# Kernel optimization log

Measured on AMD Instinct MI355X. Metric: run time of the kernel, lower is better.

Reference implementation:

```python
import jax, jax.numpy as jnp
import numpy as np

B, T, S, E, H, F = 4, 1024, 1024, 512, 8, 2048
D = E // H  # head_dim = 64
SCALE = D ** -0.5
EPS = 1e-5


def setup_inputs() -> dict:
    key = jax.random.key(0)
    ks = jax.random.split(key, 16)
    w = lambda k, shape: jax.random.normal(k, shape, jnp.float32) * 0.02
    inp = {
        'tgt': jax.random.normal(ks[0], (B, T, E), jnp.float32),
        'memory': jax.random.normal(ks[1], (B, S, E), jnp.float32),
    }
    for i, n in enumerate(['sWq', 'sWk', 'sWv', 'sWo', 'cWq', 'cWk', 'cWv', 'cWo']):
        inp[n] = w(ks[2 + i], (E, E))
    for n in ['sbq', 'sbk', 'sbv', 'sbo', 'cbq', 'cbk', 'cbv', 'cbo']:
        inp[n] = jnp.zeros((E,), jnp.float32)
    inp['fW1'] = w(ks[10], (E, F)); inp['fb1'] = jnp.zeros((F,), jnp.float32)
    inp['fW2'] = w(ks[11], (F, E)); inp['fb2'] = jnp.zeros((E,), jnp.float32)
    for n in ['g1', 'g2', 'g3']:
        inp[n] = jnp.ones((E,), jnp.float32)
    for n in ['be1', 'be2', 'be3']:
        inp[n] = jnp.zeros((E,), jnp.float32)
    return inp


def _ln(x, g, b):
    mu = jnp.mean(x, axis=-1, keepdims=True)
    var = jnp.mean(jnp.square(x - mu), axis=-1, keepdims=True)
    return (x - mu) * jax.lax.rsqrt(var + EPS) * g + b


def _mha(xq, xkv, Wq, bq, Wk, bk, Wv, bv, Wo, bo):
    # dense-equivalent of full N^2 edge-list attention (softmax over source nodes per target)
    Bq, Tq, _ = xq.shape
    Skv = xkv.shape[1]
    q = (xq @ Wq + bq).reshape(Bq, Tq, H, D)
    k = (xkv @ Wk + bk).reshape(Bq, Skv, H, D)
    v = (xkv @ Wv + bv).reshape(Bq, Skv, H, D)
    scores = jnp.einsum('bthd,bshd->bhts', q, k) * SCALE
    wts = jax.nn.softmax(scores, axis=-1)
    out = jnp.einsum('bhts,bshd->bthd', wts, v).reshape(Bq, Tq, E)
    return out @ Wo + bo


def reference(tgt, memory,
              sWq, sbq, sWk, sbk, sWv, sbv, sWo, sbo,
              cWq, cbq, cWk, cbk, cWv, cbv, cWo, cbo,
              fW1, fb1, fW2, fb2,
              g1, be1, g2, be2, g3, be3):
    # post-norm decoder layer: self-attn -> cross-attn -> FFN (dropout=0 eval)
    x = _ln(tgt + _mha(tgt, tgt, sWq, sbq, sWk, sbk, sWv, sbv, sWo, sbo), g1, be1)
    x = _ln(x + _mha(x, memory, cWq, cbq, cWk, cbk, cWv, cbv, cWo, cbo), g2, be2)
    ff = jax.nn.relu(x @ fW1 + fb1) @ fW2 + fb2
    x = _ln(x + ff, g3, be3)
    return x
```

## Files before the change

### kernel.cpp

```cpp
#include <hip/hip_runtime.h>

typedef unsigned short ushort_t;
typedef short short8 __attribute__((ext_vector_type(8)));
typedef float float4v __attribute__((ext_vector_type(4)));

__device__ __forceinline__ float bf2f(ushort_t u) {
    union { unsigned int i; float f; } x; x.i = ((unsigned int)u) << 16; return x.f;
}
__device__ __forceinline__ ushort_t f2bf(float f) {
    unsigned int u = __float_as_uint(f);
    unsigned int r = (u + 0x7FFFu + ((u >> 16) & 1u)) >> 16;
    return (ushort_t)r;
}
__device__ __forceinline__ void store_out(float* p, float v) { *p = v; }
__device__ __forceinline__ void store_out(ushort_t* p, float v) { *p = f2bf(v); }

__device__ __forceinline__ void gll16(const ushort_t* g, ushort_t* l) {
    __builtin_amdgcn_global_load_lds(
        (const __attribute__((address_space(1))) void*)g,
        (__attribute__((address_space(3))) void*)l, 16, 0, 0);
}

__global__ void detect_dtype(const ushort_t* __restrict__ tgt, int* __restrict__ flag) {
    __shared__ int red[256];
    const int tid = threadIdx.x;
    int p = 0;
    for (int i = tid; i < 512; i += 256) {
        ushort_t u = tgt[i];
        int e = (u >> 7) & 0xFF;
        if (u == 0 || (e >= 100 && e <= 140)) ++p;
    }
    red[tid] = p; __syncthreads();
    for (int off = 128; off > 0; off >>= 1) {
        if (tid < off) red[tid] += red[tid + off];
        __syncthreads();
    }
    if (tid == 0) flag[0] = (red[0] >= 480) ? 1 : 0;
}

__global__ __launch_bounds__(256) void prep_all(
    const void* sWq, const void* sWk, const void* sWv, const void* sWo,
    const void* cWq, const void* cWk, const void* cWv, const void* cWo,
    const void* fW1, const void* fW2,
    const void* tgt, const void* mem,
    const void* sbq, const void* sbk, const void* sbv, const void* sbo,
    const void* cbq, const void* cbk, const void* cbv, const void* cbo,
    const void* fb1, const void* fb2,
    ushort_t* __restrict__ wb, ushort_t* __restrict__ tb, ushort_t* __restrict__ mb,
    float* __restrict__ pb, const int* __restrict__ dflag)
{
    const bool f32 = (dflag[0] == 0);
    const int tid = threadIdx.x;
    const int z = blockIdx.z;

    if (z < 10) {
        const void* src; ushort_t* dst; int Kd, Nd;
        switch (z) {
            case 0: src = sWq; dst = wb + 0;       Kd = 512;  Nd = 512;  break;
            case 1: src = sWk; dst = wb + 262144;  Kd = 512;  Nd = 512;  break;
            case 2: src = sWv; dst = wb + 524288;  Kd = 512;  Nd = 512;  break;
            case 3: src = sWo; dst = wb + 786432;  Kd = 512;  Nd = 512;  break;
            case 4: src = cWq; dst = wb + 1048576; Kd = 512;  Nd = 512;  break;
            case 5: src = cWk; dst = wb + 1310720; Kd = 512;  Nd = 512;  break;
            case 6: src = cWv; dst = wb + 1572864; Kd = 512;  Nd = 512;  break;
            case 7: src = cWo; dst = wb + 1835008; Kd = 512;  Nd = 512;  break;
            case 8: src = fW1; dst = wb + 2097152; Kd = 512;  Nd = 2048; break;
            default:src = fW2; dst = wb + 3145728; Kd = 2048; Nd = 512;  break;
        }
        const int k0 = blockIdx.x * 64, n0 = blockIdx.y * 64;
        if (k0 >= Kd || n0 >= Nd) return;
        __shared__ ushort_t T[64][65];
#pragma unroll
        for (int i = 0; i < 16; ++i) {
            int j = i * 256 + tid;
            int r = j >> 6, c = j & 63;
            float v = f32 ? ((const float*)src)[(size_t)(k0 + r) * Nd + n0 + c]
                          : bf2f(((const ushort_t*)src)[(size_t)(k0 + r) * Nd + n0 + c]);
            T[r][c] = f2bf(v);
        }
        __syncthreads();
#pragma unroll
        for (int i = 0; i < 16; ++i) {
            int j = i * 256 + tid;
            int n = j >> 6, k = j & 63;
            dst[(size_t)(n0 + n) * Kd + k0 + k] = T[k][n];
        }
        return;
    }

    const int bid = blockIdx.x * 32 + blockIdx.y;
    if (z < 12) {
        const void* src = (z == 10) ? tgt : mem;
        ushort_t* dst = (z == 10) ? tb : mb;
        const int i = (bid * 256 + tid) * 8;
        if (f32) {
            float4 v0 = *(const float4*)((const float*)src + i);
            float4 v1 = *(const float4*)((const float*)src + i + 4);
            ushort_t o[8] = { f2bf(v0.x), f2bf(v0.y), f2bf(v0.z), f2bf(v0.w),
                              f2bf(v1.x), f2bf(v1.y), f2bf(v1.z), f2bf(v1.w) };
            *(uint4*)(dst + i) = *(const uint4*)o;
        } else {
            *(uint4*)(dst + i) = *(const uint4*)((const ushort_t*)src + i);
        }
        return;
    }

    {
        const int i = bid * 256 + tid;
        if (bid >= 26 || i >= 6656) return;
        const void* src; int off;
        if      (i < 512)  { src = sbq; off = i; }
        else if (i < 1024) { src = sbk; off = i - 512; }
        else if (i < 1536) { src = sbv; off = i - 1024; }
        else if (i < 2048) { src = sbo; off = i - 1536; }
        else if (i < 2560) { src = cbq; off = i - 2048; }
        else if (i < 3072) { src = cbk; off = i - 2560; }
        else if (i < 3584) { src = cbv; off = i - 3072; }
        else if (i < 4096) { src = cbo; off = i - 3584; }
        else if (i < 6144) { src = fb1; off = i - 4096; }
        else               { src = fb2; off = i - 6144; }
        pb[i] = f32 ? ((const float*)src)[off] : bf2f(((const ushort_t*)src)[off]);
    }
}

template<typename OutT, bool RELU, int BN>
__global__ __launch_bounds__(256) void gemm_tn(
    const ushort_t* __restrict__ A1, const ushort_t* __restrict__ A2,
    int ySplit, int lda,
    const ushort_t* __restrict__ Wt, int ldw,
    const float* __restrict__ bias,
    OutT* __restrict__ C, int ldc, int K)
{
    constexpr int MI = (BN == 128) ? 4 : 2;
    __shared__ ushort_t As[2][128][32];
    __shared__ ushort_t Bs[2][BN][32];
    const int tid = threadIdx.x;
    const int wave = tid >> 6, lane = tid & 63;
    const int quad = lane >> 4, l16 = lane & 15;
    const int m0 = blockIdx.x * 128, n0 = blockIdx.y * BN;
    const int wm = (BN == 128) ? (wave >> 1) * 64 : wave * 32;
    const int wn = (BN == 128) ? (wave & 1) * 64 : 0;
    const ushort_t* A = (((int)blockIdx.y) < ySplit) ? A1 : A2;

    float4v acc[MI][4];
#pragma unroll
    for (int mi = 0; mi < MI; ++mi)
#pragma unroll
        for (int ni = 0; ni < 4; ++ni) {
            acc[mi][ni][0] = 0.f; acc[mi][ni][1] = 0.f;
            acc[mi][ni][2] = 0.f; acc[mi][ni][3] = 0.f;
        }

    const int srow = lane >> 2;
    const int scc  = lane & 3;
    const int sg   = (scc - (lane >> 3)) & 3;
    const ushort_t* aptr0 = A  + (size_t)(m0 + wave * 16 + srow) * lda + sg * 8;
    const ushort_t* aptr1 = A  + (size_t)(m0 + 64 + wave * 16 + srow) * lda + sg * 8;
    const ushort_t* bptr0 = Wt + (size_t)(n0 + wave * 16 + srow) * ldw + sg * 8;
    const ushort_t* bptr1 = Wt + (size_t)(n0 + 64 + wave * 16 + srow) * ldw + sg * 8;

    gll16(aptr0, &As[0][wave * 16][0]);
    gll16(aptr1, &As[0][64 + wave * 16][0]);
    gll16(bptr0, &Bs[0][wave * 16][0]);
    if (BN == 128) gll16(bptr1, &Bs[0][64 + wave * 16][0]);

    const int ca = ((quad + (l16 >> 1)) & 3) * 8;
    int cur = 0;
    for (int k0 = 0; k0 < K; k0 += 32) {
        __syncthreads();
        if (k0 + 32 < K) {
            const int nb = cur ^ 1, ko = k0 + 32;
            gll16(aptr0 + ko, &As[nb][wave * 16][0]);
            gll16(aptr1 + ko, &As[nb][64 + wave * 16][0]);
            gll16(bptr0 + ko, &Bs[nb][wave * 16][0]);
            if (BN == 128) gll16(bptr1 + ko, &Bs[nb][64 + wave * 16][0]);
        }
        short8 af[MI], bfr[4];
#pragma unroll
        for (int mi = 0; mi < MI; ++mi)
            af[mi] = *(const short8*)(&As[cur][wm + mi * 16 + l16][ca]);
#pragma unroll
        for (int ni = 0; ni < 4; ++ni)
            bfr[ni] = *(const short8*)(&Bs[cur][wn + ni * 16 + l16][ca]);
#pragma unroll
        for (int mi = 0; mi < MI; ++mi)
#pragma unroll
            for (int ni = 0; ni < 4; ++ni)
                acc[mi][ni] = __builtin_amdgcn_mfma_f32_16x16x32_bf16(
                    af[mi], bfr[ni], acc[mi][ni], 0, 0, 0);
        cur ^= 1;
    }

#pragma unroll
    for (int ni = 0; ni < 4; ++ni) {
        const int col = n0 + wn + ni * 16 + l16;
        const float bv = bias[col];
#pragma unroll
        for (int mi = 0; mi < MI; ++mi)
#pragma unroll
            for (int r = 0; r < 4; ++r) {
                const int row = m0 + wm + mi * 16 + quad * 4 + r;
                float v = acc[mi][ni][r] + bv;
                if (RELU) v = fmaxf(v, 0.f);
                store_out(&C[(size_t)row * ldc + col], v);
            }
    }
}

__global__ __launch_bounds__(512) void attn_mfma(ushort_t* __restrict__ QKV)
{
    const int S = 1536;
    __shared__ ushort_t PsA[64][72];
    __shared__ ushort_t PsB[64][72];
    __shared__ ushort_t Ks[2][64][72];
    __shared__ ushort_t Vt[2][64][72];

    const int tid  = threadIdx.x;
    const int w    = tid >> 6;
    const int g    = w >> 2;
    const int wq   = w & 3;
    const int lane = tid & 63;
    const int quad = lane >> 4, l16 = lane & 15;
    const int ht   = tid & 255;
    const int qt = blockIdx.x, bh = blockIdx.y;
    const int b = bh >> 3, h = bh & 7;
    const size_t rowQ = (size_t)b * 1024 + qt * 64;
    const size_t kv0  = (size_t)b * 1024;

    const int kr = ht >> 2, kc = (ht & 3) * 16;
    const int sp = ht >> 3, dc = (ht & 7) * 8;
    const int vr0 = sp * 2;
    const int vrg = vr0 >> 3, vrof = vr0 & 7;

    {
        const int r = tid >> 3, c = (tid & 7) * 8;
        *(uint4*)(&PsA[r][c]) = *(const uint4*)(QKV + (rowQ + r) * S + h * 64 + c);
    }
    __syncthreads();
    short8 qf[2];
    qf[0] = *(const short8*)(&PsA[wq * 16 + l16][quad * 8]);
    qf[1] = *(const short8*)(&PsA[wq * 16 + l16][32 + quad * 8]);
    ushort_t (* __restrict__ Ps)[72] = g ? PsB : PsA;

    const float CEXP = 0.125f * 1.44269504f;
    const float MREF = 16.0f * CEXP;
    float lsum[4];
    float4v oacc[4];
#pragma unroll
    for (int r = 0; r < 4; ++r) lsum[r] = 0.f;
#pragma unroll
    for (int n = 0; n < 4; ++n) { oacc[n][0]=0.f; oacc[n][1]=0.f; oacc[n][2]=0.f; oacc[n][3]=0.f; }

    uint4 kA, kB, vA, vB;
    {
        const size_t sr = kv0 + g * 64;
        const ushort_t* ksrc = QKV + (sr + kr) * S + 512 + h * 64 + kc;
        kA = *(const uint4*)(ksrc);
        kB = *(const uint4*)(ksrc + 8);
        const ushort_t* vsrc = QKV + (sr + vr0) * S + 1024 + h * 64 + dc;
        vA = *(const uint4*)(vsrc);
        vB = *(const uint4*)(vsrc + S);
    }

    for (int it = 0; it < 8; ++it) {
        __syncthreads();
        *(uint4*)(&Ks[g][kr][kc])     = kA;
        *(uint4*)(&Ks[g][kr][kc + 8]) = kB;
        {
            const ushort_t* ae = (const ushort_t*)&vA;
            const ushort_t* be = (const ushort_t*)&vB;
#pragma unroll
            for (int j = 0; j < 8; ++j) {
                const int d = dc + j;
                const int cc = (vrg ^ (d >> 4)) & 7;
                *(unsigned int*)(&Vt[g][d][cc * 8 + vrof]) =
                    (unsigned int)ae[j] | ((unsigned int)be[j] << 16);
            }
        }
        __syncthreads();
        if (it < 7) {
            const size_t sr = kv0 + (it + 1) * 128 + g * 64;
            const ushort_t* ksrc = QKV + (sr + kr) * S + 512 + h * 64 + kc;
            kA = *(const uint4*)(ksrc);
            kB = *(const uint4*)(ksrc + 8);
            const ushort_t* vsrc = QKV + (sr + vr0) * S + 1024 + h * 64 + dc;
            vA = *(const uint4*)(vsrc);
            vB = *(const uint4*)(vsrc + S);
        }

        float4v sc[4];
#pragma unroll
        for (int sb = 0; sb < 4; ++sb) {
            float4v z; z[0]=0.f; z[1]=0.f; z[2]=0.f; z[3]=0.f;
            short8 kf0 = *(const short8*)(&Ks[g][sb * 16 + l16][quad * 8]);
            short8 kf1 = *(const short8*)(&Ks[g][sb * 16 + l16][32 + quad * 8]);
            z = __builtin_amdgcn_mfma_f32_16x16x32_bf16(qf[0], kf0, z, 0, 0, 0);
            z = __builtin_amdgcn_mfma_f32_16x16x32_bf16(qf[1], kf1, z, 0, 0, 0);
            sc[sb] = z;
        }

#pragma unroll
        for (int sb = 0; sb < 4; ++sb)
#pragma unroll
            for (int r = 0; r < 4; ++r) {
                float p = exp2f(fmaf(sc[sb][r], CEXP, -MREF));
                lsum[r] += p;
                Ps[wq * 16 + quad * 4 + r][sb * 16 + l16] = f2bf(p);
            }

        short8 pf[2];
        pf[0] = *(const short8*)(&Ps[wq * 16 + l16][quad * 8]);
        pf[1] = *(const short8*)(&Ps[wq * 16 + l16][32 + quad * 8]);
#pragma unroll
        for (int n = 0; n < 4; ++n) {
#pragma unroll
            for (int kc2 = 0; kc2 < 2; ++kc2) {
                const int cc = ((kc2 * 4 + quad) ^ n) & 7;
                short8 vf = *(const short8*)(&Vt[g][n * 16 + l16][cc * 8]);
                oacc[n] = __builtin_amdgcn_mfma_f32_16x16x32_bf16(pf[kc2], vf, oacc[n], 0, 0, 0);
            }
        }
    }

#pragma unroll
    for (int msk = 1; msk < 16; msk <<= 1)
#pragma unroll
        for (int r = 0; r < 4; ++r) lsum[r] += __shfl_xor(lsum[r], msk);

    float* exch = (float*)&Ks[0][0][0];
    float* exl  = (float*)&Vt[0][0][0];
    __syncthreads();
    if (g == 1) {
#pragma unroll
        for (int n = 0; n < 4; ++n)
#pragma unroll
            for (int r = 0; r < 4; ++r)
                exch[((wq * 4 + n) * 4 + r) * 64 + lane] = oacc[n][r];
        if (l16 == 0)
#pragma unroll
            for (int r = 0; r < 4; ++r) exl[wq * 16 + quad * 4 + r] = lsum[r];
    }
    __syncthreads();
    if (g == 0) {
#pragma unroll
        for (int r = 0; r < 4; ++r) lsum[r] += exl[wq * 16 + quad * 4 + r];
        float inv[4];
#pragma unroll
        for (int r = 0; r < 4; ++r) inv[r] = 1.f / lsum[r];
#pragma unroll
        for (int n = 0; n < 4; ++n)
#pragma unroll
            for (int r = 0; r < 4; ++r) {
                float o = oacc[n][r] + exch[((wq * 4 + n) * 4 + r) * 64 + lane];
                const size_t row = rowQ + wq * 16 + quad * 4 + r;
                QKV[row * S + h * 64 + n * 16 + l16] = f2bf(o * inv[r]);
            }
    }
}

template<bool RES_EXT, bool DELTA_F32, bool OUT_FLAG>
__global__ __launch_bounds__(256) void ln_kernel(
    const void* __restrict__ res, const void* __restrict__ delta,
    const void* __restrict__ g, const void* __restrict__ be,
    void* __restrict__ out, const int* __restrict__ dflag)
{
    const int E = 512;
    const bool extf32 = (dflag[0] == 0);
    const int row = blockIdx.x, tid = threadIdx.x;
    const int wave = tid >> 6, lane = tid & 63;
    const size_t base = (size_t)row * E;
    const int i0 = tid, i1 = tid + 256;

    float r0, r1;
    if (RES_EXT && extf32) {
        r0 = ((const float*)res)[base + i0];
        r1 = ((const float*)res)[base + i1];
    } else {
        r0 = bf2f(((const ushort_t*)res)[base + i0]);
        r1 = bf2f(((const ushort_t*)res)[base + i1]);
    }
    float d0v, d1v;
    if (DELTA_F32) {
        d0v = ((const float*)delta)[base + i0];
        d1v = ((const float*)delta)[base + i1];
    } else {
        d0v = bf2f(((const ushort_t*)delta)[base + i0]);
        d1v = bf2f(((const ushort_t*)delta)[base + i1]);
    }
    float x0 = r0 + d0v, x1 = r1 + d1v;

    __shared__ float red8[8];
    float s = x0 + x1;
#pragma unroll
    for (int m = 1; m < 64; m <<= 1) s += __shfl_xor(s, m);
    if (lane == 0) red8[wave] = s;
    __syncthreads();
    float mean = (red8[0] + red8[1] + red8[2] + red8[3]) * (1.0f / 512.0f);
    float dd0 = x0 - mean, dd1 = x1 - mean;
    float v = dd0 * dd0 + dd1 * dd1;
#pragma unroll
    for (int m = 1; m < 64; m <<= 1) v += __shfl_xor(v, m);
    if (lane == 0) red8[4 + wave] = v;
    __syncthreads();
    float rstd = rsqrtf((red8[4] + red8[5] + red8[6] + red8[7]) * (1.0f / 512.0f) + 1e-5f);

    float g0, g1v, b0, b1;
    if (extf32) {
        g0 = ((const float*)g)[i0];  g1v = ((const float*)g)[i1];
        b0 = ((const float*)be)[i0]; b1  = ((const float*)be)[i1];
    } else {
        g0 = bf2f(((const ushort_t*)g)[i0]);  g1v = bf2f(((const ushort_t*)g)[i1]);
        b0 = bf2f(((const ushort_t*)be)[i0]); b1  = bf2f(((const ushort_t*)be)[i1]);
    }
    float y0 = dd0 * rstd * g0 + b0;
    float y1 = dd1 * rstd * g1v + b1;
    if (OUT_FLAG && extf32) {
        ((float*)out)[base + i0] = y0; ((float*)out)[base + i1] = y1;
    } else {
        ((ushort_t*)out)[base + i0] = f2bf(y0);
        ((ushort_t*)out)[base + i1] = f2bf(y1);
    }
}


extern "C" void kernel_launch(void* const* d_in, const int* in_sizes, int n_in,
                              void* d_out, int out_size, void* d_ws, size_t ws_size,
                              hipStream_t stream) {
    const void* tgt = d_in[0];
    const void* mem = d_in[1];
    const void* sWq = d_in[2];  const void* sWk = d_in[3];
    const void* sWv = d_in[4];  const void* sWo = d_in[5];
    const void* cWq = d_in[6];  const void* cWk = d_in[7];
    const void* cWv = d_in[8];  const void* cWo = d_in[9];
    const void* sbq = d_in[10]; const void* sbk = d_in[11];
    const void* sbv = d_in[12]; const void* sbo = d_in[13];
    const void* cbq = d_in[14]; const void* cbk = d_in[15];
    const void* cbv = d_in[16]; const void* cbo = d_in[17];
    const void* fW1 = d_in[18]; const void* fb1 = d_in[19];
    const void* fW2 = d_in[20]; const void* fb2 = d_in[21];
    const void* g1  = d_in[22]; const void* g2  = d_in[23];
    const void* g3  = d_in[24];
    const void* be1 = d_in[25]; const void* be2 = d_in[26];
    const void* be3 = d_in[27];

    char* ws = (char*)d_ws;
    const size_t MB = 1048576;
    ushort_t* qkv = (ushort_t*)(ws + 0 * MB);
    ushort_t* hb  = (ushort_t*)(ws + 0 * MB);
    ushort_t* po  = (ushort_t*)(ws + 12 * MB);
    ushort_t* xb  = (ushort_t*)(ws + 16 * MB);
    ushort_t* tb  = (ushort_t*)(ws + 20 * MB);
    ushort_t* mb  = (ushort_t*)(ws + 24 * MB);
    float*    of  = (float*)   (ws + 20 * MB);
    ushort_t* wb  = (ushort_t*)(ws + 28 * MB);
    float*    pb  = (float*)   (ws + 36 * MB);
    int*   dflag  = (int*)     (ws + 36 * MB + 262144);

    const ushort_t* sWqkv_t = wb + 0;
    const ushort_t* sWo_t   = wb + 786432;
    const ushort_t* cWqkv_t = wb + 1048576;
    const ushort_t* cWo_t   = wb + 1835008;
    const ushort_t* fW1_t   = wb + 2097152;
    const ushort_t* fW2_t   = wb + 3145728;

    dim3 blk(256);

    detect_dtype<<<dim3(1), blk, 0, stream>>>((const ushort_t*)tgt, dflag);
    prep_all<<<dim3(32, 32, 13), blk, 0, stream>>>(
        sWq, sWk, sWv, sWo, cWq, cWk, cWv, cWo, fW1, fW2,
        tgt, mem, sbq, sbk, sbv, sbo, cbq, cbk, cbv, cbo, fb1, fb2,
        wb, tb, mb, pb, dflag);

    dim3 gattn(16, 32);
    dim3 blk512(512);

    gemm_tn<ushort_t, false, 128><<<dim3(32, 12), blk, 0, stream>>>(tb, tb, 0, 512, sWqkv_t, 512, pb + 0, qkv, 1536, 512);
    attn_mfma<<<gattn, blk512, 0, stream>>>(qkv);
    gemm_tn<ushort_t, false, 64><<<dim3(32, 8), blk, 0, stream>>>(qkv, qkv, 0, 1536, sWo_t, 512, pb + 1536, po, 512, 512);
    ln_kernel<true, false, false><<<dim3(4096), blk, 0, stream>>>(tgt, po, g1, be1, xb, dflag);

    gemm_tn<ushort_t, false, 128><<<dim3(32, 12), blk, 0, stream>>>(xb, mb, 4, 512, cWqkv_t, 512, pb + 2048, qkv, 1536, 512);
    attn_mfma<<<gattn, blk512, 0, stream>>>(qkv);
    gemm_tn<ushort_t, false, 64><<<dim3(32, 8), blk, 0, stream>>>(qkv, qkv, 0, 1536, cWo_t, 512, pb + 3584, po, 512, 512);
    ln_kernel<false, false, false><<<dim3(4096), blk, 0, stream>>>(xb, po, g2, be2, xb, dflag);

    gemm_tn<ushort_t, true, 128><<<dim3(32, 16), blk, 0, stream>>>(xb, xb, 0, 512, fW1_t, 512, pb + 4096, hb, 2048, 512);
    gemm_tn<float, false, 64><<<dim3(32, 8), blk, 0, stream>>>(hb, hb, 0, 2048, fW2_t, 2048, pb + 6144, of, 512, 2048);
    ln_kernel<false, true, true><<<dim3(4096), blk, 0, stream>>>(xb, of, g3, be3, d_out, dflag);
}
```

Baseline: 306.8 us.

## Split-K output projections into two bf16 partials summed in layernorm

The output-projection and FFN-down GEMMs are split along K into two halves over gridDim.z. Each half writes a bf16 partial, and the following layernorm kernel adds the two partials. This doubles the block count on these small 256-block GEMMs to fill more CUs, at the cost of extra partial traffic and bf16 rounding of the partials (the FFN2 output was fp32 before). Also, the dtype is inferred from input sizes so the detect kernel is skipped, and prep_all uses a compact 1D grid instead of a mostly-idle 3D grid.

```diff
diff --git a/kernel.cpp b/kernel.cpp
--- a/kernel.cpp
+++ b/kernel.cpp
@@ -36,6 +36,10 @@
         __syncthreads();
     }
     if (tid == 0) flag[0] = (red[0] >= 480) ? 1 : 0;
+}
+
+__device__ __forceinline__ bool is_f32(int mode, const int* dflag) {
+    return (mode == 2) ? (dflag[0] == 0) : (mode == 0);
 }
 
 __global__ __launch_bounds__(256) void prep_all(
@@ -47,13 +51,17 @@
     const void* cbq, const void* cbk, const void* cbv, const void* cbo,
     const void* fb1, const void* fb2,
     ushort_t* __restrict__ wb, ushort_t* __restrict__ tb, ushort_t* __restrict__ mb,
-    float* __restrict__ pb, const int* __restrict__ dflag)
+    float* __restrict__ pb, int mode, const int* __restrict__ dflag)
 {
-    const bool f32 = (dflag[0] == 0);
+    const bool f32 = is_f32(mode, dflag);
     const int tid = threadIdx.x;
-    const int z = blockIdx.z;
-
-    if (z < 10) {
+    const int id = blockIdx.x;
+
+    if (id < 1024) {
+        int z, kt, nt;
+        if (id < 512)      { z = id >> 6;  int t = id & 63;  kt = t >> 3; nt = t & 7;  }
+        else if (id < 768) { z = 8;        int t = id - 512; kt = t >> 5; nt = t & 31; }
+        else               { z = 9;        int t = id - 768; kt = t >> 3; nt = t & 7;  }
         const void* src; ushort_t* dst; int Kd, Nd;
         switch (z) {
             case 0: src = sWq; dst = wb + 0;       Kd = 512;  Nd = 512;  break;
@@ -67,8 +75,7 @@
             case 8: src = fW1; dst = wb + 2097152; Kd = 512;  Nd = 2048; break;
             default:src = fW2; dst = wb + 3145728; Kd = 2048; Nd = 512;  break;
         }
-        const int k0 = blockIdx.x * 64, n0 = blockIdx.y * 64;
-        if (k0 >= Kd || n0 >= Nd) return;
+        const int k0 = kt * 64, n0 = nt * 64;
         __shared__ ushort_t T[64][65];
 #pragma unroll
         for (int i = 0; i < 16; ++i) {
@@ -88,10 +95,11 @@
         return;
     }
 
-    const int bid = blockIdx.x * 32 + blockIdx.y;
-    if (z < 12) {
-        const void* src = (z == 10) ? tgt : mem;
-        ushort_t* dst = (z == 10) ? tb : mb;
+    if (id < 3072) {
+        const int bid0 = id - 1024;
+        const void* src = (bid0 < 1024) ? tgt : mem;
+        ushort_t* dst = (bid0 < 1024) ? tb : mb;
+        const int bid = bid0 & 1023;
         const int i = (bid * 256 + tid) * 8;
         if (f32) {
             float4 v0 = *(const float4*)((const float*)src + i);
@@ -106,8 +114,8 @@
     }
 
     {
-        const int i = bid * 256 + tid;
-        if (bid >= 26 || i >= 6656) return;
+        const int i = (id - 3072) * 256 + tid;
+        if (i >= 6656) return;
         const void* src; int off;
         if      (i < 512)  { src = sbq; off = i; }
         else if (i < 1024) { src = sbk; off = i - 512; }
@@ -123,13 +131,14 @@
     }
 }
 
-template<typename OutT, bool RELU, int BN>
+template<typename OutT, bool RELU, int BN, bool KSPLIT>
 __global__ __launch_bounds__(256) void gemm_tn(
     const ushort_t* __restrict__ A1, const ushort_t* __restrict__ A2,
     int ySplit, int lda,
     const ushort_t* __restrict__ Wt, int ldw,
     const float* __restrict__ bias,
-    OutT* __restrict__ C, int ldc, int K)
+    OutT* __restrict__ C, int ldc, int K,
+    OutT* __restrict__ C2)
 {
     constexpr int MI = (BN == 128) ? 4 : 2;
     __shared__ ushort_t As[2][128][32];
@@ -141,6 +150,10 @@
     const int wm = (BN == 128) ? (wave >> 1) * 64 : wave * 32;
     const int wn = (BN == 128) ? (wave & 1) * 64 : 0;
     const ushort_t* A = (((int)blockIdx.y) < ySplit) ? A1 : A2;
+    const ushort_t* W = Wt;
+    OutT* Cw = C;
+    bool second = false;
+    if (KSPLIT && blockIdx.z) { A += K; W += K; Cw = C2; second = true; }
 
     float4v acc[MI][4];
 #pragma unroll
@@ -156,8 +169,8 @@
     const int sg   = (scc - (lane >> 3)) & 3;
     const ushort_t* aptr0 = A  + (size_t)(m0 + wave * 16 + srow) * lda + sg * 8;
     const ushort_t* aptr1 = A  + (size_t)(m0 + 64 + wave * 16 + srow) * lda + sg * 8;
-    const ushort_t* bptr0 = Wt + (size_t)(n0 + wave * 16 + srow) * ldw + sg * 8;
-    const ushort_t* bptr1 = Wt + (size_t)(n0 + 64 + wave * 16 + srow) * ldw + sg * 8;
+    const ushort_t* bptr0 = W + (size_t)(n0 + wave * 16 + srow) * ldw + sg * 8;
+    const ushort_t* bptr1 = W + (size_t)(n0 + 64 + wave * 16 + srow) * ldw + sg * 8;
 
     gll16(aptr0, &As[0][wave * 16][0]);
     gll16(aptr1, &As[0][64 + wave * 16][0]);
@@ -194,7 +207,7 @@
 #pragma unroll
     for (int ni = 0; ni < 4; ++ni) {
         const int col = n0 + wn + ni * 16 + l16;
-        const float bv = bias[col];
+        const float bv = (KSPLIT && second) ? 0.f : bias[col];
 #pragma unroll
         for (int mi = 0; mi < MI; ++mi)
 #pragma unroll
@@ -202,7 +215,7 @@
                 const int row = m0 + wm + mi * 16 + quad * 4 + r;
                 float v = acc[mi][ni][r] + bv;
                 if (RELU) v = fmaxf(v, 0.f);
-                store_out(&C[(size_t)row * ldc + col], v);
+                store_out(&Cw[(size_t)row * ldc + col], v);
             }
     }
 }
@@ -358,14 +371,15 @@
     }
 }
 
-template<bool RES_EXT, bool DELTA_F32, bool OUT_FLAG>
+template<bool RES_EXT, bool OUT_EXT>
 __global__ __launch_bounds__(256) void ln_kernel(
-    const void* __restrict__ res, const void* __restrict__ delta,
+    const void* __restrict__ res,
+    const ushort_t* __restrict__ d1, const ushort_t* __restrict__ d2,
     const void* __restrict__ g, const void* __restrict__ be,
-    void* __restrict__ out, const int* __restrict__ dflag)
+    void* __restrict__ out, int mode, const int* __restrict__ dflag)
 {
     const int E = 512;
-    const bool extf32 = (dflag[0] == 0);
+    const bool extf32 = is_f32(mode, dflag);
     const int row = blockIdx.x, tid = threadIdx.x;
     const int wave = tid >> 6, lane = tid & 63;
     const size_t base = (size_t)row * E;
@@ -379,14 +393,8 @@
         r0 = bf2f(((const ushort_t*)res)[base + i0]);
         r1 = bf2f(((const ushort_t*)res)[base + i1]);
     }
-    float d0v, d1v;
-    if (DELTA_F32) {
-        d0v = ((const float*)delta)[base + i0];
-        d1v = ((const float*)delta)[base + i1];
-    } else {
-        d0v = bf2f(((const ushort_t*)delta)[base + i0]);
-        d1v = bf2f(((const ushort_t*)delta)[base + i1]);
-    }
+    float d0v = bf2f(d1[base + i0]) + bf2f(d2[base + i0]);
+    float d1v = bf2f(d1[base + i1]) + bf2f(d2[base + i1]);
     float x0 = r0 + d0v, x1 = r1 + d1v;
 
     __shared__ float red8[8];
@@ -414,7 +422,7 @@
     }
     float y0 = dd0 * rstd * g0 + b0;
     float y1 = dd1 * rstd * g1v + b1;
-    if (OUT_FLAG && extf32) {
+    if (OUT_EXT && extf32) {
         ((float*)out)[base + i0] = y0; ((float*)out)[base + i1] = y1;
     } else {
         ((ushort_t*)out)[base + i0] = f2bf(y0);
@@ -447,11 +455,13 @@
     const size_t MB = 1048576;
     ushort_t* qkv = (ushort_t*)(ws + 0 * MB);
     ushort_t* hb  = (ushort_t*)(ws + 0 * MB);
-    ushort_t* po  = (ushort_t*)(ws + 12 * MB);
+    ushort_t* pA  = (ushort_t*)(ws + 12 * MB);
     ushort_t* xb  = (ushort_t*)(ws + 16 * MB);
     ushort_t* tb  = (ushort_t*)(ws + 20 * MB);
     ushort_t* mb  = (ushort_t*)(ws + 24 * MB);
-    float*    of  = (float*)   (ws + 20 * MB);
+    ushort_t* pB  = (ushort_t*)(ws + 20 * MB);
+    ushort_t* ofA = (ushort_t*)(ws + 20 * MB);
+    ushort_t* ofB = (ushort_t*)(ws + 24 * MB);
     ushort_t* wb  = (ushort_t*)(ws + 28 * MB);
     float*    pb  = (float*)   (ws + 36 * MB);
     int*   dflag  = (int*)     (ws + 36 * MB + 262144);
@@ -465,26 +475,41 @@
 
     dim3 blk(256);
 
-    detect_dtype<<<dim3(1), blk, 0, stream>>>((const ushort_t*)tgt, dflag);
-    prep_all<<<dim3(32, 32, 13), blk, 0, stream>>>(
+    int mode;
+    if (in_sizes[0] == 4 * 1024 * 512 * 4)      mode = 0;
+    else if (in_sizes[0] == 4 * 1024 * 512 * 2) mode = 1;
+    else                                        mode = 2;
+    if (mode == 2)
+        detect_dtype<<<dim3(1), blk, 0, stream>>>((const ushort_t*)tgt, dflag);
+
+    prep_all<<<dim3(3098), blk, 0, stream>>>(
         sWq, sWk, sWv, sWo, cWq, cWk, cWv, cWo, fW1, fW2,
         tgt, mem, sbq, sbk, sbv, sbo, cbq, cbk, cbv, cbo, fb1, fb2,
-        wb, tb, mb, pb, dflag);
+        wb, tb, mb, pb, mode, dflag);
 
     dim3 gattn(16, 32);
     dim3 blk512(512);
 
-    gemm_tn<ushort_t, false, 128><<<dim3(32, 12), blk, 0, stream>>>(tb, tb, 0, 512, sWqkv_t, 512, pb + 0, qkv, 1536, 512);
+    gemm_tn<ushort_t, false, 128, false><<<dim3(32, 12), blk, 0, stream>>>(
+        tb, tb, 0, 512, sWqkv_t, 512, pb + 0, qkv, 1536, 512, (ushort_t*)nullptr);
     attn_mfma<<<gattn, blk512, 0, stream>>>(qkv);
-    gemm_tn<ushort_t, false, 64><<<dim3(32, 8), blk, 0, stream>>>(qkv, qkv, 0, 1536, sWo_t, 512, pb + 1536, po, 512, 512);
-    ln_kernel<true, false, false><<<dim3(4096), blk, 0, stream>>>(tgt, po, g1, be1, xb, dflag);
-
-    gemm_tn<ushort_t, false, 128><<<dim3(32, 12), blk, 0, stream>>>(xb, mb, 4, 512, cWqkv_t, 512, pb + 2048, qkv, 1536, 512);
+    gemm_tn<ushort_t, false, 64, true><<<dim3(32, 8, 2), blk, 0, stream>>>(
+        qkv, qkv, 0, 1536, sWo_t, 512, pb + 1536, pA, 512, 256, pB);
+    ln_kernel<true, false><<<dim3(4096), blk, 0, stream>>>(
+        tgt, pA, pB, g1, be1, xb, mode, dflag);
+
+    gemm_tn<ushort_t, false, 128, false><<<dim3(32, 12), blk, 0, stream>>>(
+        xb, mb, 4, 512, cWqkv_t, 512, pb + 2048, qkv, 1536, 512, (ushort_t*)nullptr);
     attn_mfma<<<gattn, blk512, 0, stream>>>(qkv);
-    gemm_tn<ushort_t, false, 64><<<dim3(32, 8), blk, 0, stream>>>(qkv, qkv, 0, 1536, cWo_t, 512, pb + 3584, po, 512, 512);
-    ln_kernel<false, false, false><<<dim3(4096), blk, 0, stream>>>(xb, po, g2, be2, xb, dflag);
-
-    gemm_tn<ushort_t, true, 128><<<dim3(32, 16), blk, 0, stream>>>(xb, xb, 0, 512, fW1_t, 512, pb + 4096, hb, 2048, 512);
-    gemm_tn<float, false, 64><<<dim3(32, 8), blk, 0, stream>>>(hb, hb, 0, 2048, fW2_t, 2048, pb + 6144, of, 512, 2048);
-    ln_kernel<false, true, true><<<dim3(4096), blk, 0, stream>>>(xb, of, g3, be3, d_out, dflag);
-}
+    gemm_tn<ushort_t, false, 64, true><<<dim3(32, 8, 2), blk, 0, stream>>>(
+        qkv, qkv, 0, 1536, cWo_t, 512, pb + 3584, pA, 512, 256, pB);
+    ln_kernel<false, false><<<dim3(4096), blk, 0, stream>>>(
+        xb, pA, pB, g2, be2, xb, mode, dflag);
+
+    gemm_tn<ushort_t, true, 128, false><<<dim3(32, 16), blk, 0, stream>>>(
+        xb, xb, 0, 512, fW1_t, 512, pb + 4096, hb, 2048, 512, (ushort_t*)nullptr);
+    gemm_tn<ushort_t, false, 64, true><<<dim3(32, 8, 2), blk, 0, stream>>>(
+        hb, hb, 0, 2048, fW2_t, 2048, pb + 6144, ofA, 512, 1024, ofB);
+    ln_kernel<false, true><<<dim3(4096), blk, 0, stream>>>(
+        xb, ofA, ofB, g3, be3, d_out, mode, dflag);
+}
```

New measurement: 280.2 us. -8.7%, faster.
